# Kernel optimization log

Hardware: AMD Instinct MI355X
Metric: run time of the kernel (lower is better)

The kernel has to match this reference:

```python
import jax, jax.numpy as jnp
import numpy as np
import math

B, L, D = 4, 4096, 1024
PI = math.pi
LN_EPS = 1e-5


def setup_inputs() -> dict:
    key = jax.random.key(0)
    ks = jax.random.split(key, 16)
    s = 1.0 / math.sqrt(D)
    inp = {
        "x": jax.random.normal(ks[0], (B, L, D), dtype=jnp.float32),
        # Linear weights stored as [in, out] (torch W.T)
        "Wk": jax.random.normal(ks[1], (D, D), dtype=jnp.float32) * s,
        "bk": jnp.zeros((D,), dtype=jnp.float32),
        "Wq": jax.random.normal(ks[2], (D, D), dtype=jnp.float32) * s,
        "bq": jnp.zeros((D,), dtype=jnp.float32),
        "Wv": jax.random.normal(ks[3], (D, D), dtype=jnp.float32) * s,
        "bv": jnp.zeros((D,), dtype=jnp.float32),
        "ln_g": jnp.ones((D,), dtype=jnp.float32),
        "ln_b": jnp.zeros((D,), dtype=jnp.float32),
        "Wo": jax.random.normal(ks[4], (D, D), dtype=jnp.float32) * s,
        "bo": jnp.zeros((D,), dtype=jnp.float32),
        "Wg1": jax.random.normal(ks[5], (D, D // 4), dtype=jnp.float32) * s,
        "bg1": jnp.zeros((D // 4,), dtype=jnp.float32),
        "Wg2": jax.random.normal(ks[6], (D // 4, 1), dtype=jnp.float32) * (2.0 / math.sqrt(D)),
        "bg2": jnp.zeros((1,), dtype=jnp.float32),
        "pos_phases": jax.random.normal(ks[7], (L, D), dtype=jnp.float32) * PI,
    }
    return inp


def _layernorm(x, g, b):
    mu = jnp.mean(x, axis=-1, keepdims=True)
    var = jnp.var(x, axis=-1, keepdims=True)
    return (x - mu) * jax.lax.rsqrt(var + LN_EPS) * g + b


def reference(x, Wk, bk, Wq, bq, Wv, bv, ln_g, ln_b, Wo, bo, Wg1, bg1, Wg2, bg2, pos_phases):
    # dropout is identity in eval mode
    key_phases = jnp.tanh(x @ Wk + bk) * PI          # [B,L,D]
    query_phases = jnp.tanh(x @ Wq + bq) * PI        # [B,L,D]
    V = x @ Wv + bv                                   # [B,L,D]

    cos_k, sin_k = jnp.cos(key_phases), jnp.sin(key_phases)
    cos_q, sin_q = jnp.cos(query_phases), jnp.sin(query_phases)

    mem_real = jnp.cumsum(V * cos_k, axis=1)
    mem_imag = jnp.cumsum(V * sin_k, axis=1)
    content_retrieved = mem_real * cos_q + mem_imag * sin_q

    pp = pos_phases[: x.shape[1]]                     # [L,D]
    cos_p, sin_p = jnp.cos(pp), jnp.sin(pp)
    pos_mem_real = jnp.cumsum(V * cos_p, axis=1)
    pos_mem_imag = jnp.cumsum(V * sin_p, axis=1)
    pos_retrieved = pos_mem_real * cos_p + pos_mem_imag * sin_p

    gate = jax.nn.sigmoid(jax.nn.gelu(x @ Wg1 + bg1) @ Wg2 + bg2)  # [B,L,1]
    combined = gate * content_retrieved + (1.0 - gate) * pos_retrieved

    positions = jnp.arange(1, x.shape[1] + 1, dtype=jnp.float32)
    norm = jnp.sqrt(positions)[None, :, None]
    out = _layernorm(combined / norm, ln_g, ln_b) @ Wo + bo
    return x + out
```

## Files before the change

kernel.cpp:

```cpp
#include <hip/hip_runtime.h>
#include <math.h>

#define B_ 4
#define L_ 4096
#define D_ 1024
#define DG_ 256
#define NC_ 128
#define CL_ 32
#define PI_F 3.14159265358979323846f
#define LN_EPS_F 1e-5f

typedef __attribute__((ext_vector_type(8))) _Float16 f16x8;
typedef __attribute__((ext_vector_type(8))) short s16x8;
typedef __attribute__((ext_vector_type(4))) short s16x4;
typedef __attribute__((ext_vector_type(4))) float f32x4;

__device__ inline short f2h(float f) { return __builtin_bit_cast(short, (_Float16)f); }
__device__ inline float h2f(short s) { return (float)__builtin_bit_cast(_Float16, s); }

__device__ inline float ftanh(float x) {
    float e = __expf(2.0f * x);
    return 1.0f - 2.0f / (e + 1.0f);
}
__device__ inline void fsincos(float x, float* s, float* c) {
    *s = __sinf(x); *c = __cosf(x);
}

__device__ inline void gld16(const void* g, void* l) {
    __builtin_amdgcn_global_load_lds(
        (const __attribute__((address_space(1))) unsigned int*)g,
        (__attribute__((address_space(3))) unsigned int*)l, 16, 0, 0);
}

__global__ __launch_bounds__(256)
void conv_x(const float* __restrict__ x, short* __restrict__ xh, int n8)
{
    int t = blockIdx.x * 256 + threadIdx.x;
    if (t >= n8) return;
    const float4* p = (const float4*)x + (size_t)t * 2;
    float4 a = p[0], b = p[1];
    s16x8 v;
    v[0] = f2h(a.x); v[1] = f2h(a.y); v[2] = f2h(a.z); v[3] = f2h(a.w);
    v[4] = f2h(b.x); v[5] = f2h(b.y); v[6] = f2h(b.z); v[7] = f2h(b.w);
    *(s16x8*)(xh + (size_t)t * 8) = v;
}

__global__ __launch_bounds__(256)
void convT(const float* __restrict__ W, short* __restrict__ Th, int N)
{
    __shared__ float tile[64][65];
    const int n0 = blockIdx.x * 64, k0 = blockIdx.y * 64;
    const int t = threadIdx.x;
    const int r = t >> 4, c4 = (t & 15) * 4;

    #pragma unroll
    for (int i = 0; i < 4; ++i) {
        float4 v = *(const float4*)&W[(size_t)(k0 + r + i * 16) * N + n0 + c4];
        tile[r + i * 16][c4 + 0] = v.x;
        tile[r + i * 16][c4 + 1] = v.y;
        tile[r + i * 16][c4 + 2] = v.z;
        tile[r + i * 16][c4 + 3] = v.w;
    }
    __syncthreads();
    #pragma unroll
    for (int i = 0; i < 4; ++i) {
        const int n = r + i * 16;
        s16x4 o;
        o[0] = f2h(tile[c4 + 0][n]);
        o[1] = f2h(tile[c4 + 1][n]);
        o[2] = f2h(tile[c4 + 2][n]);
        o[3] = f2h(tile[c4 + 3][n]);
        *(s16x4*)&Th[(size_t)(n0 + n) * 1024 + k0 + c4] = o;
    }
}

#define SBAR() __builtin_amdgcn_sched_barrier(0)
#define BARRIER() do { SBAR(); __builtin_amdgcn_s_barrier(); SBAR(); } while (0)
#define LDH(P, IMM) (*(const f16x8*)((P) + (IMM)))

#define RD_AF(BASEIMM)                                                  \
    _Pragma("unroll") for (int i_ = 0; i_ < 4; ++i_) {                  \
        af[i_][0] = LDH(Ak0, (BASEIMM) + i_ * 2048);                    \
        af[i_][1] = LDH(Ak1, (BASEIMM) + i_ * 2048);                    \
    }
#define RD_BQ(BASEIMM)                                                  \
    _Pragma("unroll") for (int n_ = 0; n_ < 4; ++n_) {                  \
        bq[n_][0] = LDH(Bk0, (BASEIMM) + n_ * 2048);                    \
        bq[n_][1] = LDH(Bk1, (BASEIMM) + n_ * 2048);                    \
    }
#define MFMAS(MG)                                                       \
    _Pragma("unroll") for (int i_ = 0; i_ < 4; ++i_)                    \
    _Pragma("unroll") for (int n_ = 0; n_ < 4; ++n_)                    \
    _Pragma("unroll") for (int kk_ = 0; kk_ < 2; ++kk_)                 \
        acc[(MG) * 4 + i_][n_] = __builtin_amdgcn_mfma_f32_16x16x32_f16(\
            af[i_][kk_], bq[n_][kk_], acc[(MG) * 4 + i_][n_], 0, 0, 0);

template<int EPI, typename OT>
__global__ __launch_bounds__(512, 2)
void mgemm256(const short* __restrict__ A, const short* __restrict__ Bt,
              const float* __restrict__ X, OT* __restrict__ out0,
              short* __restrict__ out1, short* __restrict__ out2,
              const float* __restrict__ b0, const float* __restrict__ b1,
              const float* __restrict__ b2, int M, int N, int K)
{
    extern __shared__ char lds[];

    const int tid = threadIdx.x;
    const int w = tid >> 6, l = tid & 63;
    const int wr = w >> 2, wc = w & 3;
    const int fr = l & 15, kb = l >> 4;
    const int bm = blockIdx.x * 256, bn = blockIdx.y * 256;
    const int np = K >> 7;

    const int s = fr & 7;
    const int cK0 = (((s >> 2) & 1) << 6) | (((kb ^ s) & 3) << 4);
    const char* Ak0 = lds + (wr << 14) + fr * 128 + cK0;
    const char* Ak1 = lds + (wr << 14) + fr * 128 + (cK0 ^ 64);
    const char* Bk0 = lds + 32768 + ((wc >> 1) << 14) + ((wc & 1) * 64 + fr) * 128 + cK0;
    const char* Bk1 = lds + 32768 + ((wc >> 1) << 14) + ((wc & 1) * 64 + fr) * 128 + (cK0 ^ 64);

    const int p0 = tid * 16;
    const int sr = p0 >> 7;
    const int sc = (p0 & 127) ^ ((sr & 7) << 4);
    const short* gA = A  + (size_t)(bm + sr) * K + (sc >> 1);
    const short* gB = Bt + (size_t)(bn + sr) * K + (sc >> 1);
    char* ldst = lds + (w << 10);
    const size_t q1 = (size_t)64 * K, q2 = 2 * q1, q3 = 3 * q1;

    f32x4 acc[8][4] = {};
    f16x8 af[4][2];
    f16x8 bq[4][2];

    gld16(gA,       ldst);
    gld16(gA + q1,  ldst + 8192);
    gld16(gA + q2,  ldst + 16384);
    gld16(gA + q3,  ldst + 24576);
    gld16(gB,       ldst + 32768);
    gld16(gB + q1,  ldst + 40960);
    gld16(gB + q2,  ldst + 49152);
    gld16(gB + q3,  ldst + 57344);
    gld16(gA +      64, ldst + 65536);
    gld16(gA + q2 + 64, ldst + 65536 + 16384);
    asm volatile("s_waitcnt vmcnt(2)" ::: "memory");
    BARRIER();

    const short* gA1 = gA + 64;
    const short* gB1 = gB + 64;

    for (int pp = 0; pp < np; ++pp) {
        const bool nl = (pp + 1 < np);

        RD_AF(0); RD_BQ(0);
        gld16(gA1 + q1, ldst + 65536 + 8192);
        gld16(gA1 + q3, ldst + 65536 + 24576);
        gld16(gB1,      ldst + 65536 + 32768);
        gld16(gB1 + q1, ldst + 65536 + 40960);
        BARRIER();
        __builtin_amdgcn_s_setprio(1); MFMAS(0); __builtin_amdgcn_s_setprio(0);
        BARRIER();
        RD_AF(8192);
        gld16(gB1 + q2, ldst + 65536 + 49152);
        gld16(gB1 + q3, ldst + 65536 + 57344);
        if (nl) {
            gld16(gA1 +      64, ldst);
            gld16(gA1 + q2 + 64, ldst + 16384);
        }
        BARRIER();
        __builtin_amdgcn_s_setprio(1); MFMAS(1); __builtin_amdgcn_s_setprio(0);
        SBAR();
        if (nl) asm volatile("s_waitcnt vmcnt(2)" ::: "memory");
        else    asm volatile("s_waitcnt vmcnt(0)" ::: "memory");
        __builtin_amdgcn_s_barrier(); SBAR();

        RD_AF(65536); RD_BQ(65536);
        if (nl) {
            gld16(gA1 + q1 + 64, ldst + 8192);
            gld16(gA1 + q3 + 64, ldst + 24576);
            gld16(gB1 +      64, ldst + 32768);
            gld16(gB1 + q1 + 64, ldst + 40960);
        }
        BARRIER();
        __builtin_amdgcn_s_setprio(1); MFMAS(0); __builtin_amdgcn_s_setprio(0);
        BARRIER();
        RD_AF(65536 + 8192);
        if (nl) {
            gld16(gB1 + q2 + 64, ldst + 49152);
            gld16(gB1 + q3 + 64, ldst + 57344);
            gld16(gA1 +      128, ldst + 65536);
            gld16(gA1 + q2 + 128, ldst + 65536 + 16384);
        }
        BARRIER();
        __builtin_amdgcn_s_setprio(1); MFMAS(1); __builtin_amdgcn_s_setprio(0);
        SBAR();
        if (nl) {
            asm volatile("s_waitcnt vmcnt(2)" ::: "memory");
            __builtin_amdgcn_s_barrier(); SBAR();
        }
        gA1 += 128; gB1 += 128;
    }

    if constexpr (EPI == 4) {
        short* op; const float* bp; bool dt;
        if (bn < 1024)      { op = (short*)out0; bp = b0; dt = true;  }
        else if (bn < 2048) { op = out1;         bp = b1; dt = true;  }
        else                { op = out2;         bp = b2; dt = false; }
        const int cb = bn & 1023;
        #pragma unroll
        for (int nf = 0; nf < 4; ++nf) {
            const int cc = cb + wc * 64 + nf * 16 + fr;
            const float bcol = bp[cc];
            #pragma unroll
            for (int mf = 0; mf < 8; ++mf)
                #pragma unroll
                for (int rr = 0; rr < 4; ++rr) {
                    const int row = bm + wr * 128 + mf * 16 + kb * 4 + rr;
                    float c = acc[mf][nf][rr] + bcol;
                    if (dt) c = ftanh(c) * PI_F;
                    op[(size_t)row * 1024 + cc] = f2h(c);
                }
        }
    } else {
        #pragma unroll
        for (int nf = 0; nf < 4; ++nf) {
            const int col = bn + wc * 64 + nf * 16 + fr;
            const float bcol = b0[col];
            #pragma unroll
            for (int mf = 0; mf < 8; ++mf)
                #pragma unroll
                for (int rr = 0; rr < 4; ++rr) {
                    const int row = bm + wr * 128 + mf * 16 + kb * 4 + rr;
                    float c = acc[mf][nf][rr] + bcol + X[(size_t)row * N + col];
                    ((float*)out0)[(size_t)row * N + col] = c;
                }
        }
    }
}

template<int EPI>
__global__ __launch_bounds__(256)
void mgemm(const short* __restrict__ A, const short* __restrict__ Bt,
           short* __restrict__ out0, const float* __restrict__ b0,
           int M, int N, int K)
{
    __shared__ __align__(16) short As[128 * 32];
    __shared__ __align__(16) short Bs[128 * 32];

    const int tid = threadIdx.x;
    const int w  = tid >> 6, l = tid & 63;
    const int wr = w >> 1,  wc = w & 1;
    const int fr = l & 15,  kb = l >> 4;
    const int bm = blockIdx.x * 128, bn = blockIdx.y * 128;

    const int srow = l >> 2;
    const int scol = (l & 3) * 8;
    const short* gA0 = A  + (size_t)(bm + w * 32 +  0 + srow) * K + scol;
    const short* gA1 = A  + (size_t)(bm + w * 32 + 16 + srow) * K + scol;
    const short* gB0 = Bt + (size_t)(bn + w * 32 +  0 + srow) * K + scol;
    const short* gB1 = Bt + (size_t)(bn + w * 32 + 16 + srow) * K + scol;
    short* lA0 = &As[(w * 32 +  0) * 32];
    short* lA1 = &As[(w * 32 + 16) * 32];
    short* lB0 = &Bs[(w * 32 +  0) * 32];
    short* lB1 = &Bs[(w * 32 + 16) * 32];

    f32x4 acc[4][4] = {};

    for (int k0 = 0; k0 < K; k0 += 32) {
        gld16(gA0 + k0, lA0); gld16(gA1 + k0, lA1);
        gld16(gB0 + k0, lB0); gld16(gB1 + k0, lB1);
        __syncthreads();

        f16x8 afr[4], bfr[4];
        #pragma unroll
        for (int m = 0; m < 4; ++m)
            afr[m] = *(const f16x8*)&As[(wr * 64 + m * 16 + fr) * 32 + kb * 8];
        #pragma unroll
        for (int n = 0; n < 4; ++n)
            bfr[n] = *(const f16x8*)&Bs[(wc * 64 + n * 16 + fr) * 32 + kb * 8];
        #pragma unroll
        for (int m = 0; m < 4; ++m)
            #pragma unroll
            for (int n = 0; n < 4; ++n)
                acc[m][n] = __builtin_amdgcn_mfma_f32_16x16x32_f16(afr[m], bfr[n], acc[m][n], 0, 0, 0);
        __syncthreads();
    }

    #pragma unroll
    for (int n = 0; n < 4; ++n) {
        const int col = bn + wc * 64 + n * 16 + fr;
        const float bcol = b0[col];
        #pragma unroll
        for (int m = 0; m < 4; ++m)
            #pragma unroll
            for (int r = 0; r < 4; ++r) {
                const int row = bm + wr * 64 + m * 16 + kb * 4 + r;
                float c = acc[m][n][r] + bcol;
                float tt = 0.7978845608028654f * (c + 0.044715f * c * c * c);
                c = 0.5f * c * (1.0f + ftanh(tt));
                out0[(size_t)row * N + col] = f2h(c);
            }
    }
}

__global__ __launch_bounds__(256)
void gate_kernel(const short* __restrict__ H, const float* __restrict__ Wg2,
                 const float* __restrict__ bg2, float* __restrict__ gate)
{
    const int wid = threadIdx.x >> 6;
    const int lane = threadIdx.x & 63;
    const int row = blockIdx.x * 4 + wid;
    s16x4 hv = *(const s16x4*)&H[(size_t)row * DG_ + lane * 4];
    float4 wv = *(const float4*)&Wg2[lane * 4];
    float s = h2f(hv[0]) * wv.x + h2f(hv[1]) * wv.y + h2f(hv[2]) * wv.z + h2f(hv[3]) * wv.w;
    #pragma unroll
    for (int o = 32; o; o >>= 1) s += __shfl_down(s, o);
    if (lane == 0) gate[row] = 1.0f / (1.0f + __expf(-(s + bg2[0])));
}

__global__ __launch_bounds__(256)
void passA(const short* __restrict__ V, const short* __restrict__ KP,
           const float* __restrict__ PP, f32x4* __restrict__ SI)
{
    const int bid = blockIdx.x;
    const int b = bid >> 7, c = bid & 127;
    const int d0 = threadIdx.x * 4;

    f32x4 cr = {}, ci = {}, pr = {}, pi = {};
    const size_t base  = ((size_t)b * L_ + (size_t)c * CL_) * D_ + d0;
    const size_t pbase = (size_t)c * CL_ * D_ + d0;
    for (int ll = 0; ll < CL_; ++ll) {
        s16x4 v4  = *(const s16x4*)&V [base + (size_t)ll * D_];
        s16x4 kp4 = *(const s16x4*)&KP[base + (size_t)ll * D_];
        f32x4 pp4 = *(const f32x4*)&PP[pbase + (size_t)ll * D_];
        #pragma unroll
        for (int j = 0; j < 4; ++j) {
            float v = h2f(v4[j]);
            float sk, ck, sp, cp;
            fsincos(h2f(kp4[j]), &sk, &ck);
            fsincos(pp4[j], &sp, &cp);
            cr[j] += v * ck; ci[j] += v * sk;
            pr[j] += v * cp; pi[j] += v * sp;
        }
    }
    const size_t sidx = ((size_t)bid << 10) + d0;
    #pragma unroll
    for (int j = 0; j < 4; ++j) {
        f32x4 o = { cr[j], ci[j], pr[j], pi[j] };
        SI[sidx + j] = o;
    }
}

__global__ __launch_bounds__(256)
void passB(f32x4* __restrict__ SI)
{
    const int t = blockIdx.x * 256 + threadIdx.x;
    const int b = t >> 10, d = t & 1023;
    f32x4 run = {};
    for (int c = 0; c < NC_; ++c) {
        const size_t idx = ((size_t)(b * NC_ + c) << 10) + d;
        f32x4 v = SI[idx];
        SI[idx] = run;
        run += v;
    }
}

__global__ __launch_bounds__(256)
void passC(const short* __restrict__ V, const short* KP,
           const short* __restrict__ QP, const float* __restrict__ PP,
           const float* __restrict__ gate, const f32x4* __restrict__ SI,
           const float* __restrict__ ln_g, const float* __restrict__ ln_b,
           short* Yb)
{
    const int bid = blockIdx.x;
    const int b = bid >> 7, c = bid & 127;
    const int d0 = threadIdx.x * 4;

    const size_t sidx = ((size_t)bid << 10) + d0;
    f32x4 cr, ci, pr, pi;
    #pragma unroll
    for (int j = 0; j < 4; ++j) {
        f32x4 s = SI[sidx + j];
        cr[j] = s[0]; ci[j] = s[1]; pr[j] = s[2]; pi[j] = s[3];
    }
    const f32x4 g_ln = *(const f32x4*)&ln_g[d0];
    const f32x4 b_ln = *(const f32x4*)&ln_b[d0];

    __shared__ float2 lred[2][4];
    const int wid = threadIdx.x >> 6;
    const int lane = threadIdx.x & 63;

    for (int l0 = 0; l0 < CL_; ++l0) {
        const int ll = c * CL_ + l0;
        const size_t off = ((size_t)b * L_ + ll) * D_ + d0;
        s16x4 v4  = *(const s16x4*)&V [off];
        s16x4 kp4 = *(const s16x4*)&KP[off];
        s16x4 qp4 = *(const s16x4*)&QP[off];
        f32x4 pp4 = *(const f32x4*)&PP[(size_t)ll * D_ + d0];
        const float gv = gate[b * L_ + ll];
        const float rs_pos = rsqrtf((float)(ll + 1));

        f32x4 u;
        #pragma unroll
        for (int j = 0; j < 4; ++j) {
            float v = h2f(v4[j]);
            float sk, ck, sq, cq, sp, cp;
            fsincos(h2f(kp4[j]), &sk, &ck);
            fsincos(h2f(qp4[j]), &sq, &cq);
            fsincos(pp4[j], &sp, &cp);
            cr[j] += v * ck; ci[j] += v * sk;
            pr[j] += v * cp; pi[j] += v * sp;
            float content = cr[j] * cq + ci[j] * sq;
            float posr    = pr[j] * cp + pi[j] * sp;
            u[j] = (gv * content + (1.0f - gv) * posr) * rs_pos;
        }

        float s  = u[0] + u[1] + u[2] + u[3];
        float s2 = u[0]*u[0] + u[1]*u[1] + u[2]*u[2] + u[3]*u[3];
        #pragma unroll
        for (int o = 32; o; o >>= 1) {
            s  += __shfl_down(s, o);
            s2 += __shfl_down(s2, o);
        }
        const int pb = l0 & 1;
        if (lane == 0) lred[pb][wid] = make_float2(s, s2);
        __syncthreads();
        float ts  = lred[pb][0].x + lred[pb][1].x + lred[pb][2].x + lred[pb][3].x;
        float ts2 = lred[pb][0].y + lred[pb][1].y + lred[pb][2].y + lred[pb][3].y;
        const float mu  = ts * (1.0f / D_);
        const float var = ts2 * (1.0f / D_) - mu * mu;
        const float rsv = rsqrtf(var + LN_EPS_F);
        s16x4 yo;
        #pragma unroll
        for (int j = 0; j < 4; ++j)
            yo[j] = f2h((u[j] - mu) * rsv * g_ln[j] + b_ln[j]);
        *(s16x4*)&Yb[off] = yo;
    }
}

extern "C" void kernel_launch(void* const* d_in, const int* in_sizes, int n_in,
                              void* d_out, int out_size, void* d_ws, size_t ws_size,
                              hipStream_t stream)
{
    const float* x    = (const float*)d_in[0];
    const float* Wk   = (const float*)d_in[1];
    const float* bk   = (const float*)d_in[2];
    const float* Wq   = (const float*)d_in[3];
    const float* bq   = (const float*)d_in[4];
    const float* Wv   = (const float*)d_in[5];
    const float* bv   = (const float*)d_in[6];
    const float* ln_g = (const float*)d_in[7];
    const float* ln_b = (const float*)d_in[8];
    const float* Wo   = (const float*)d_in[9];
    const float* bo   = (const float*)d_in[10];
    const float* Wg1  = (const float*)d_in[11];
    const float* bg1  = (const float*)d_in[12];
    const float* Wg2  = (const float*)d_in[13];
    const float* bg2  = (const float*)d_in[14];
    const float* PP   = (const float*)d_in[15];

    float* out = (float*)d_out;

    const size_t BLD   = (size_t)B_ * L_ * D_;
    const size_t SZ_X  = BLD * 2;
    const size_t SZ_R1 = (size_t)B_ * L_ * DG_ * 2;
    const size_t SZ_G1 = (size_t)D_ * DG_ * 2;
    const size_t NEED  = SZ_X + SZ_R1 + SZ_G1 + 3 * SZ_X;
    if (ws_size < NEED) {
        hipMemcpyAsync(d_out, d_in[0], BLD * sizeof(float),
                       hipMemcpyDeviceToDevice, stream);
        return;
    }

    char* wsb = (char*)d_ws;
    short* xh   = (short*)(wsb);
    char*  r1   = wsb + SZ_X;
    short* Wcat = (short*)r1;
    short* H    = (short*)r1;
    short* Wg1T = (short*)(r1 + SZ_R1);
    short* KP   = (short*)(r1 + SZ_R1 + SZ_G1);
    short* QP   = (short*)((char*)KP + SZ_X);
    short* V    = (short*)((char*)QP + SZ_X);
    float* gate = (float*)(wsb);
    short* WtO  = (short*)(wsb + 65536);
    f32x4* SI   = (f32x4*)(wsb + 65536 + 2097152);
    short* Yb   = KP;

    const int M = B_ * L_;
    dim3 blk(256);

    conv_x<<<(int)(BLD / 8 / 256), blk, 0, stream>>>(x, xh, (int)(BLD / 8));
    dim3 gT(D_ / 64, 16);
    dim3 gTg(DG_ / 64, 16);
    convT<<<gT, blk, 0, stream>>>(Wk, Wcat + 0 * D_ * D_, D_);
    convT<<<gT, blk, 0, stream>>>(Wq, Wcat + 1 * D_ * D_, D_);
    convT<<<gT, blk, 0, stream>>>(Wv, Wcat + 2 * D_ * D_, D_);
    convT<<<gTg, blk, 0, stream>>>(Wg1, Wg1T, DG_);

    dim3 gQKV(M / 256, 3072 / 256);
    dim3 gH(M / 128, DG_ / 128);
    hipLaunchKernelGGL((mgemm256<4, short>), gQKV, dim3(512), 131072, stream,
                       xh, Wcat, nullptr, KP, QP, V, bk, bq, bv, M, 3072, D_);
    hipLaunchKernelGGL((mgemm<2>), gH, blk, 0, stream,
                       xh, Wg1T, H, bg1, M, DG_, D_);

    gate_kernel<<<M / 4, blk, 0, stream>>>(H, Wg2, bg2, gate);
    convT<<<gT, blk, 0, stream>>>(Wo, WtO, D_);

    passA<<<B_ * NC_, blk, 0, stream>>>(V, KP, PP, SI);
    passB<<<(B_ * D_) / 256, blk, 0, stream>>>(SI);
    passC<<<B_ * NC_, blk, 0, stream>>>(V, KP, QP, PP, gate, SI, ln_g, ln_b, Yb);

    dim3 gO(M / 256, D_ / 256);
    hipLaunchKernelGGL((mgemm256<3, float>), gO, dim3(512), 131072, stream,
                       Yb, WtO, x, out, nullptr, nullptr, bo, nullptr, nullptr,
                       M, D_, D_);
}
```

Measured before the change: 326.1 us.

## Split GEMM main loop into finer k-halves to cut register pressure

Restructures the software-pipelined MFMA loop in the 256x256 GEMM so each phase loads and computes one k-half (KK) at a time. The A fragment register array drops from two halves to one. There are now twice as many compute phases, separated by barriers, and the global-to-LDS prefetches are re-sequenced, including a new B staging offset at 98304. The aim is to lower VGPR use and interleave LDS reads with MFMA more finely, at the cost of extra barriers and a changed vmcnt wait ordering.

```diff
diff --git a/kernel.cpp b/kernel.cpp
--- a/kernel.cpp
+++ b/kernel.cpp
@@ -76,24 +76,21 @@
 
 #define SBAR() __builtin_amdgcn_sched_barrier(0)
 #define BARRIER() do { SBAR(); __builtin_amdgcn_s_barrier(); SBAR(); } while (0)
+#define PRIO1() __builtin_amdgcn_s_setprio(1)
+#define PRIO0() __builtin_amdgcn_s_setprio(0)
 #define LDH(P, IMM) (*(const f16x8*)((P) + (IMM)))
 
-#define RD_AF(BASEIMM)                                                  \
-    _Pragma("unroll") for (int i_ = 0; i_ < 4; ++i_) {                  \
-        af[i_][0] = LDH(Ak0, (BASEIMM) + i_ * 2048);                    \
-        af[i_][1] = LDH(Ak1, (BASEIMM) + i_ * 2048);                    \
-    }
-#define RD_BQ(BASEIMM)                                                  \
-    _Pragma("unroll") for (int n_ = 0; n_ < 4; ++n_) {                  \
-        bq[n_][0] = LDH(Bk0, (BASEIMM) + n_ * 2048);                    \
-        bq[n_][1] = LDH(Bk1, (BASEIMM) + n_ * 2048);                    \
-    }
-#define MFMAS(MG)                                                       \
-    _Pragma("unroll") for (int i_ = 0; i_ < 4; ++i_)                    \
-    _Pragma("unroll") for (int n_ = 0; n_ < 4; ++n_)                    \
-    _Pragma("unroll") for (int kk_ = 0; kk_ < 2; ++kk_)                 \
-        acc[(MG) * 4 + i_][n_] = __builtin_amdgcn_mfma_f32_16x16x32_f16(\
-            af[i_][kk_], bq[n_][kk_], acc[(MG) * 4 + i_][n_], 0, 0, 0);
+#define RD_A(KK, BASE)                                                   \
+    _Pragma("unroll") for (int i_ = 0; i_ < 4; ++i_)                     \
+        af[i_] = LDH((KK) ? Ak1 : Ak0, (BASE) + i_ * 2048);
+#define RD_B(KK, BASE)                                                   \
+    _Pragma("unroll") for (int n_ = 0; n_ < 4; ++n_)                     \
+        bq[n_][KK] = LDH((KK) ? Bk1 : Bk0, (BASE) + n_ * 2048);
+#define MF(MG, KK)                                                       \
+    _Pragma("unroll") for (int i_ = 0; i_ < 4; ++i_)                     \
+    _Pragma("unroll") for (int n_ = 0; n_ < 4; ++n_)                     \
+        acc[(MG)*4 + i_][n_] = __builtin_amdgcn_mfma_f32_16x16x32_f16(   \
+            af[i_], bq[n_][KK], acc[(MG)*4 + i_][n_], 0, 0, 0);
 
 template<int EPI, typename OT>
 __global__ __launch_bounds__(512, 2)
@@ -128,75 +125,79 @@
     const size_t q1 = (size_t)64 * K, q2 = 2 * q1, q3 = 3 * q1;
 
     f32x4 acc[8][4] = {};
-    f16x8 af[4][2];
+    f16x8 af[4];
     f16x8 bq[4][2];
 
-    gld16(gA,       ldst);
-    gld16(gA + q1,  ldst + 8192);
-    gld16(gA + q2,  ldst + 16384);
-    gld16(gA + q3,  ldst + 24576);
-    gld16(gB,       ldst + 32768);
-    gld16(gB + q1,  ldst + 40960);
-    gld16(gB + q2,  ldst + 49152);
-    gld16(gB + q3,  ldst + 57344);
+    gld16(gA,      ldst);          gld16(gA + q1, ldst + 8192);
+    gld16(gA + q2, ldst + 16384);  gld16(gA + q3, ldst + 24576);
+    gld16(gB,      ldst + 32768);  gld16(gB + q1, ldst + 40960);
+    gld16(gB + q2, ldst + 49152);  gld16(gB + q3, ldst + 57344);
     gld16(gA +      64, ldst + 65536);
     gld16(gA + q2 + 64, ldst + 65536 + 16384);
     asm volatile("s_waitcnt vmcnt(2)" ::: "memory");
     BARRIER();
 
-    const short* gA1 = gA + 64;
-    const short* gB1 = gB + 64;
+    const short* gAn = gA + 64;
+    const short* gBn = gB + 64;
 
     for (int pp = 0; pp < np; ++pp) {
         const bool nl = (pp + 1 < np);
 
-        RD_AF(0); RD_BQ(0);
-        gld16(gA1 + q1, ldst + 65536 + 8192);
-        gld16(gA1 + q3, ldst + 65536 + 24576);
-        gld16(gB1,      ldst + 65536 + 32768);
-        gld16(gB1 + q1, ldst + 65536 + 40960);
-        BARRIER();
-        __builtin_amdgcn_s_setprio(1); MFMAS(0); __builtin_amdgcn_s_setprio(0);
-        BARRIER();
-        RD_AF(8192);
-        gld16(gB1 + q2, ldst + 65536 + 49152);
-        gld16(gB1 + q3, ldst + 65536 + 57344);
+        RD_A(0, 0); RD_B(0, 0);
+        gld16(gBn,      ldst + 98304);         gld16(gBn + q1, ldst + 98304 + 8192);
+        gld16(gBn + q2, ldst + 98304 + 16384); gld16(gBn + q3, ldst + 98304 + 24576);
+        BARRIER();
+        PRIO1(); MF(0, 0); PRIO0();
+        BARRIER();
+        RD_A(1, 0); RD_B(1, 0);
+        gld16(gAn + q1, ldst + 65536 + 8192);
+        gld16(gAn + q3, ldst + 65536 + 24576);
+        BARRIER();
+        PRIO1(); MF(0, 1); PRIO0();
+        BARRIER();
+        RD_A(0, 8192);
+        BARRIER();
+        PRIO1(); MF(1, 0); PRIO0();
+        BARRIER();
+        RD_A(1, 8192);
+        if (nl) { gld16(gAn + 64, ldst); gld16(gAn + 64 + q2, ldst + 16384); }
+        BARRIER();
+        PRIO1(); MF(1, 1); PRIO0();
+        SBAR();
+        asm volatile("s_waitcnt vmcnt(2)" ::: "memory");
+        __builtin_amdgcn_s_barrier(); SBAR();
+
+        RD_A(0, 65536); RD_B(0, 65536);
         if (nl) {
-            gld16(gA1 +      64, ldst);
-            gld16(gA1 + q2 + 64, ldst + 16384);
-        }
-        BARRIER();
-        __builtin_amdgcn_s_setprio(1); MFMAS(1); __builtin_amdgcn_s_setprio(0);
-        SBAR();
-        if (nl) asm volatile("s_waitcnt vmcnt(2)" ::: "memory");
-        else    asm volatile("s_waitcnt vmcnt(0)" ::: "memory");
-        __builtin_amdgcn_s_barrier(); SBAR();
-
-        RD_AF(65536); RD_BQ(65536);
+            gld16(gBn +      64, ldst + 32768); gld16(gBn + q1 + 64, ldst + 40960);
+            gld16(gBn + q2 + 64, ldst + 49152); gld16(gBn + q3 + 64, ldst + 57344);
+        }
+        BARRIER();
+        PRIO1(); MF(0, 0); PRIO0();
+        BARRIER();
+        RD_A(1, 65536); RD_B(1, 65536);
         if (nl) {
-            gld16(gA1 + q1 + 64, ldst + 8192);
-            gld16(gA1 + q3 + 64, ldst + 24576);
-            gld16(gB1 +      64, ldst + 32768);
-            gld16(gB1 + q1 + 64, ldst + 40960);
-        }
-        BARRIER();
-        __builtin_amdgcn_s_setprio(1); MFMAS(0); __builtin_amdgcn_s_setprio(0);
-        BARRIER();
-        RD_AF(65536 + 8192);
-        if (nl) {
-            gld16(gB1 + q2 + 64, ldst + 49152);
-            gld16(gB1 + q3 + 64, ldst + 57344);
-            gld16(gA1 +      128, ldst + 65536);
-            gld16(gA1 + q2 + 128, ldst + 65536 + 16384);
-        }
-        BARRIER();
-        __builtin_amdgcn_s_setprio(1); MFMAS(1); __builtin_amdgcn_s_setprio(0);
+            gld16(gAn + q1 + 64, ldst + 8192);
+            gld16(gAn + q3 + 64, ldst + 24576);
+        }
+        BARRIER();
+        PRIO1(); MF(0, 1); PRIO0();
+        BARRIER();
+        if (!nl) asm volatile("s_waitcnt vmcnt(0)" ::: "memory");
+        RD_A(0, 65536 + 8192);
+        BARRIER();
+        PRIO1(); MF(1, 0); PRIO0();
+        BARRIER();
+        RD_A(1, 65536 + 8192);
+        if (nl) { gld16(gAn + 128, ldst + 65536); gld16(gAn + 128 + q2, ldst + 65536 + 16384); }
+        BARRIER();
+        PRIO1(); MF(1, 1); PRIO0();
         SBAR();
         if (nl) {
             asm volatile("s_waitcnt vmcnt(2)" ::: "memory");
             __builtin_amdgcn_s_barrier(); SBAR();
         }
-        gA1 += 128; gB1 += 128;
+        gAn += 128; gBn += 128;
     }
 
     if constexpr (EPI == 4) {
```

Measured after the change: 323.1 us. No clear change (-0.9%).
